# Performance work log

Measured on AMD Instinct MI355X. Metric: run time of the kernel, lower is better.

Reference implementation:

```python
import jax, jax.numpy as jnp
import numpy as np

B, T, D = 64, 1024, 512          # batch, tokens, embedding_dim
K = 2048                         # num_embeddings (codebook size)
COMMITMENT_COST = 0.25


def setup_inputs() -> dict:
    key = jax.random.key(0)
    k_in, k_w = jax.random.split(key)
    inputs = jax.random.normal(k_in, (B, T, D), dtype=jnp.float32)
    w = jax.random.normal(k_w, (K, D), dtype=jnp.float32)  # codebook buffer _w
    return {"inputs": inputs, "w": w}


def reference(inputs, w):
    input_shape = inputs.shape
    flat = inputs.reshape(-1, w.shape[1])                     # [N, D]
    distances = (jnp.sum(flat * flat, axis=1, keepdims=True)
                 + jnp.sum(w * w, axis=1)
                 - 2.0 * flat @ w.T)
    encoding_indices = jnp.argmin(distances, axis=1)          # [N]
    quantized = jnp.take(w, encoding_indices, axis=0).reshape(input_shape)

    # perplexity from hard assignment histogram (equiv. to mean of one-hot encodings)
    n = flat.shape[0]
    counts = jnp.zeros((w.shape[0],), dtype=jnp.float32).at[encoding_indices].add(1.0)
    avg_probs = counts / n
    perplexity = jnp.exp(-jnp.sum(avg_probs * jnp.log(avg_probs + 1e-10)))

    # commitment loss: mse(stop_grad(quantized), inputs) * cost
    q_sg = jax.lax.stop_gradient(quantized)
    loss = jnp.mean((q_sg - inputs) ** 2) * COMMITMENT_COST

    # straight-through estimator
    quantized_st = inputs + jax.lax.stop_gradient(quantized - inputs)
    return loss, quantized_st, perplexity, encoding_indices[:, None]
```

## Files before the change

### kernel.cpp

```cpp
#include <hip/hip_runtime.h>
#include <hip/hip_fp16.h>
#include <cmath>

#define NROWS  65536
#define DIM    512
#define KCODES 2048
#define NDTOT  33554432LL
#define MARGIN_P 0.0635f

typedef __attribute__((ext_vector_type(8))) _Float16 f16x8;
typedef __attribute__((ext_vector_type(4))) float f32x4;

#define KINS3(K1,K2,K3,V) do {                       \
    unsigned int _v = (V);                           \
    unsigned int _h1 = max((K1), _v); (K1) = min((K1), _v); \
    unsigned int _h2 = max((K2), _h1); (K2) = min((K2), _h1); \
    (K3) = min((K3), _h2);                           \
} while (0)

#define MRG3(A1,A2,A3,B1,B2,B3) do {                               \
    unsigned int _x1 = min((A1),(B1)), _y1 = max((A1),(B1));       \
    unsigned int _x2 = min((A2),(B2)), _y2 = max((A2),(B2));       \
    unsigned int _x3 = min((A3),(B3));                             \
    (A1) = _x1; (A2) = min(_y1,_x2);                               \
    (A3) = min(max(_y1,_x2), min(_x3,_y2));                        \
} while (0)

#define FDEC(K) (__uint_as_float(0x44800000u | ((((K) >> 11) & 0x1FFFFFu) << 2)) - 1024.f)

__global__ __launch_bounds__(256) void k_prepw(const float* __restrict__ src,
                                               char* __restrict__ dst,
                                               float* __restrict__ norms) {
    long gid = (long)blockIdx.x * 256 + threadIdx.x;
    int c  = (int)(gid >> 6);
    int k8 = (int)(gid & 63);
    const float4* s = (const float4*)(src + (size_t)c * DIM + k8 * 8);
    float4 v0 = s[0], v1 = s[1];
    float vv[8] = {v0.x, v0.y, v0.z, v0.w, v1.x, v1.y, v1.z, v1.w};
    unsigned int hw[4];
    float nrm = 0.f;
    #pragma unroll
    for (int j = 0; j < 4; ++j) {
        unsigned int h0 = __half_as_ushort(__float2half_rn(vv[2*j]));
        unsigned int h1 = __half_as_ushort(__float2half_rn(vv[2*j+1]));
        hw[j] = h0 | (h1 << 16);
        nrm = fmaf(vv[2*j], vv[2*j], nrm);
        nrm = fmaf(vv[2*j+1], vv[2*j+1], nrm);
    }
    int cb = c >> 8, fcol = (c >> 4) & 15;
    int ks32 = k8 >> 2, sub = k8 & 3;
    int l = sub * 16 + (c & 15);
    size_t off = (size_t)((cb * 16 + ks32) * 16 + fcol) * 1024 + (size_t)l * 16;
    *(uint4*)(dst + off) = make_uint4(hw[0], hw[1], hw[2], hw[3]);
    #pragma unroll
    for (int o = 32; o; o >>= 1) nrm += __shfl_xor(nrm, o, 64);
    if ((threadIdx.x & 63) == 0) norms[c] = nrm;
}

#define EPI(CB) do {                                                         \
    _Pragma("unroll") for (int fc = 0; fc < 4; ++fc) {                       \
        unsigned int col = (unsigned)((CB) * 256 + wc * 64 + fc * 16 + (lane & 15)); \
        float wnb = wnorm[col] + 1024.f;                                     \
        _Pragma("unroll") for (int fr = 0; fr < 4; ++fr) {                   \
            _Pragma("unroll") for (int reg = 0; reg < 4; ++reg) {            \
                float kd = fmaf(-2.f, acc[fr][fc][reg], wnb);                \
                unsigned int key = ((__float_as_uint(kd) << 9) & 0xFFFFF800u) | col; \
                int s = fr * 4 + reg;                                        \
                KINS3(k1[s], k2[s], k3[s], key);                             \
            }                                                                \
            acc[fr][fc] = (f32x4){0.f, 0.f, 0.f, 0.f};                       \
        }                                                                    \
    }                                                                        \
} while (0)

#define GSTEP(T, CUR0, CUR1, CUR2, CUR3, NXT0, NXT1, NXT2, NXT3) do {        \
    {                                                                        \
        const char* _n = wp + ((size_t)((T) + 1) << 14) + (size_t)(wc * 4) * 1024 + (size_t)lane * 16; \
        NXT0 = *(const f16x8*)(_n);                                          \
        NXT1 = *(const f16x8*)(_n + 1024);                                   \
        NXT2 = *(const f16x8*)(_n + 2048);                                   \
        NXT3 = *(const f16x8*)(_n + 3072);                                   \
    }                                                                        \
    {                                                                        \
        int _ks = (T) & 15;                                                  \
        unsigned _ab = (unsigned)((wr * 64 + (lane & 15)) * 1024 + _ks * 64  \
                                  + ((lane >> 4) << 4));                     \
        _ab ^= (unsigned)((lane & 7) << 4);                                  \
        const char* _a = smem + _ab;                                         \
        f16x8 _a0 = *(const f16x8*)(_a);                                     \
        f16x8 _a1 = *(const f16x8*)(_a + 16384);                             \
        f16x8 _a2 = *(const f16x8*)(_a + 32768);                             \
        f16x8 _a3 = *(const f16x8*)(_a + 49152);                             \
        acc[0][0] = __builtin_amdgcn_mfma_f32_16x16x32_f16(_a0, CUR0, acc[0][0], 0, 0, 0); \
        acc[1][0] = __builtin_amdgcn_mfma_f32_16x16x32_f16(_a1, CUR0, acc[1][0], 0, 0, 0); \
        acc[2][0] = __builtin_amdgcn_mfma_f32_16x16x32_f16(_a2, CUR0, acc[2][0], 0, 0, 0); \
        acc[3][0] = __builtin_amdgcn_mfma_f32_16x16x32_f16(_a3, CUR0, acc[3][0], 0, 0, 0); \
        acc[0][1] = __builtin_amdgcn_mfma_f32_16x16x32_f16(_a0, CUR1, acc[0][1], 0, 0, 0); \
        acc[1][1] = __builtin_amdgcn_mfma_f32_16x16x32_f16(_a1, CUR1, acc[1][1], 0, 0, 0); \
        acc[2][1] = __builtin_amdgcn_mfma_f32_16x16x32_f16(_a2, CUR1, acc[2][1], 0, 0, 0); \
        acc[3][1] = __builtin_amdgcn_mfma_f32_16x16x32_f16(_a3, CUR1, acc[3][1], 0, 0, 0); \
        acc[0][2] = __builtin_amdgcn_mfma_f32_16x16x32_f16(_a0, CUR2, acc[0][2], 0, 0, 0); \
        acc[1][2] = __builtin_amdgcn_mfma_f32_16x16x32_f16(_a1, CUR2, acc[1][2], 0, 0, 0); \
        acc[2][2] = __builtin_amdgcn_mfma_f32_16x16x32_f16(_a2, CUR2, acc[2][2], 0, 0, 0); \
        acc[3][2] = __builtin_amdgcn_mfma_f32_16x16x32_f16(_a3, CUR2, acc[3][2], 0, 0, 0); \
        acc[0][3] = __builtin_amdgcn_mfma_f32_16x16x32_f16(_a0, CUR3, acc[0][3], 0, 0, 0); \
        acc[1][3] = __builtin_amdgcn_mfma_f32_16x16x32_f16(_a1, CUR3, acc[1][3], 0, 0, 0); \
        acc[2][3] = __builtin_amdgcn_mfma_f32_16x16x32_f16(_a2, CUR3, acc[2][3], 0, 0, 0); \
        acc[3][3] = __builtin_amdgcn_mfma_f32_16x16x32_f16(_a3, CUR3, acc[3][3], 0, 0, 0); \
    }                                                                        \
    if (((T) & 15) == 15) EPI((T) >> 4);                                     \
} while (0)

__global__ __launch_bounds__(512, 1) void k_gemm(const float* __restrict__ x,
                                                 const char* __restrict__ wp,
                                                 const float* __restrict__ wnorm,
                                                 float* __restrict__ xnorm,
                                                 int* __restrict__ idxo,
                                                 int* __restrict__ cand2o,
                                                 int* __restrict__ cand3o,
                                                 float* __restrict__ bestd) {
    __shared__ char smem[131072];
    const int tid = threadIdx.x;
    const int lane = tid & 63;
    const int wid = tid >> 6;
    const int wr = wid >> 2, wc = wid & 3;
    const int rb = blockIdx.x;

    f32x4 acc[4][4];
    #pragma unroll
    for (int i = 0; i < 4; ++i)
        #pragma unroll
        for (int j = 0; j < 4; ++j) acc[i][j] = (f32x4){0.f, 0.f, 0.f, 0.f};

    unsigned int k1[16], k2[16], k3[16];
    #pragma unroll
    for (int s = 0; s < 16; ++s) { k1[s] = k2[s] = k3[s] = 0xFFFFFFFFu; }

    const float* xs = x + (size_t)rb * 128 * DIM;
    #pragma unroll
    for (int pass = 0; pass < 16; ++pass) {
        int row = pass * 8 + wid;
        const float4* src = (const float4*)(xs + (size_t)row * DIM) + lane * 2;
        float4 u0 = src[0], u1 = src[1];
        unsigned int p0 = (unsigned int)__half_as_ushort(__float2half_rn(u0.x))
                        | ((unsigned int)__half_as_ushort(__float2half_rn(u0.y)) << 16);
        unsigned int p1 = (unsigned int)__half_as_ushort(__float2half_rn(u0.z))
                        | ((unsigned int)__half_as_ushort(__float2half_rn(u0.w)) << 16);
        unsigned int p2 = (unsigned int)__half_as_ushort(__float2half_rn(u1.x))
                        | ((unsigned int)__half_as_ushort(__float2half_rn(u1.y)) << 16);
        unsigned int p3 = (unsigned int)__half_as_ushort(__float2half_rn(u1.z))
                        | ((unsigned int)__half_as_ushort(__float2half_rn(u1.w)) << 16);
        unsigned int addr = (unsigned int)(row * 1024 + lane * 16);
        addr ^= (unsigned int)((row & 7) << 4);
        *(uint4*)(smem + addr) = make_uint4(p0, p1, p2, p3);
        float nr = u0.x * u0.x;
        nr = fmaf(u0.y, u0.y, nr); nr = fmaf(u0.z, u0.z, nr); nr = fmaf(u0.w, u0.w, nr);
        nr = fmaf(u1.x, u1.x, nr); nr = fmaf(u1.y, u1.y, nr);
        nr = fmaf(u1.z, u1.z, nr); nr = fmaf(u1.w, u1.w, nr);
        #pragma unroll
        for (int o = 32; o; o >>= 1) nr += __shfl_xor(nr, o, 64);
        if (lane == 0) xnorm[rb * 128 + row] = nr;
    }
    f16x8 b0_0, b0_1, b0_2, b0_3, b1_0, b1_1, b1_2, b1_3;
    {
        const char* n0 = wp + (size_t)(wc * 4) * 1024 + (size_t)lane * 16;
        b0_0 = *(const f16x8*)(n0);
        b0_1 = *(const f16x8*)(n0 + 1024);
        b0_2 = *(const f16x8*)(n0 + 2048);
        b0_3 = *(const f16x8*)(n0 + 3072);
    }
    __syncthreads();

    for (int t = 0; t < 128; t += 2) {
        GSTEP(t,     b0_0, b0_1, b0_2, b0_3, b1_0, b1_1, b1_2, b1_3);
        GSTEP(t + 1, b1_0, b1_1, b1_2, b1_3, b0_0, b0_1, b0_2, b0_3);
    }

    #pragma unroll
    for (int s = 0; s < 16; ++s) {
        #pragma unroll
        for (int off = 1; off < 16; off <<= 1) {
            unsigned int b1 = (unsigned)__shfl_xor((int)k1[s], off, 16);
            unsigned int b2 = (unsigned)__shfl_xor((int)k2[s], off, 16);
            unsigned int b3 = (unsigned)__shfl_xor((int)k3[s], off, 16);
            MRG3(k1[s], k2[s], k3[s], b1, b2, b3);
        }
    }
    unsigned int m1 = 0, m2 = 0, m3 = 0;
    #pragma unroll
    for (int s = 0; s < 16; ++s) {
        bool mine = (lane & 15) == s;
        m1 = mine ? k1[s] : m1;
        m2 = mine ? k2[s] : m2;
        m3 = mine ? k3[s] : m3;
    }
    int sl = lane & 15;
    int rowl = wr * 64 + (sl >> 2) * 16 + (lane >> 4) * 4 + (sl & 3);
    __syncthreads();
    ((uint4*)smem)[rowl * 4 + wc] = make_uint4(m1, m2, m3, 0u);
    __syncthreads();
    if (tid < 128) {
        uint4 a = ((const uint4*)smem)[tid * 4 + 0];
        uint4 b = ((const uint4*)smem)[tid * 4 + 1];
        uint4 c = ((const uint4*)smem)[tid * 4 + 2];
        uint4 d = ((const uint4*)smem)[tid * 4 + 3];
        unsigned int K1 = a.x, K2 = a.y, K3 = a.z;
        MRG3(K1, K2, K3, b.x, b.y, b.z);
        MRG3(K1, K2, K3, c.x, c.y, c.z);
        MRG3(K1, K2, K3, d.x, d.y, d.z);
        float f1 = FDEC(K1);
        float f2 = FDEC(K2);
        float f3 = FDEC(K3);
        int row = rb * 128 + tid;
        idxo[row]   = (int)(K1 & 0x7FFu);
        bestd[row]  = f1;
        cand2o[row] = (f2 - f1 < MARGIN_P) ? (int)(K2 & 0x7FFu) : -1;
        cand3o[row] = (f3 - f1 < MARGIN_P) ? (int)(K3 & 0x7FFu) : -1;
    }
}

__global__ __launch_bounds__(256) void k_gather2(const float* __restrict__ x,
                                                 const float* __restrict__ w,
                                                 const int* __restrict__ idxo,
                                                 const int* __restrict__ cand2o,
                                                 const int* __restrict__ cand3o,
                                                 const float* __restrict__ bestd,
                                                 const float* __restrict__ xnorm,
                                                 float* __restrict__ out,
                                                 int* __restrict__ hist,
                                                 double* __restrict__ part) {
    __shared__ double red[4];
    int wid = threadIdx.x >> 6, lane = threadIdx.x & 63;
    int n = blockIdx.x * 4 + wid;
    int c1 = idxo[n];
    int c2 = cand2o[n];
    int cfin = c1;
    double dist = (double)bestd[n];
    if (c2 >= 0) {
        int c3 = cand3o[n];
        int c3e = (c3 < 0) ? c1 : c3;
        const float* xr = x + (size_t)n * DIM;
        const float* w1 = w + (size_t)c1 * DIM;
        const float* w2 = w + (size_t)c2 * DIM;
        const float* w3 = w + (size_t)c3e * DIM;
        double s1 = 0.0, s2 = 0.0, s3 = 0.0;
        #pragma unroll
        for (int j = 0; j < DIM / 64; ++j) {
            int d = lane + 64 * j;
            double xv = (double)xr[d];
            double a = (double)w1[d], b = (double)w2[d], c = (double)w3[d];
            s1 += a * a - 2.0 * xv * a;
            s2 += b * b - 2.0 * xv * b;
            s3 += c * c - 2.0 * xv * c;
        }
        #pragma unroll
        for (int off = 32; off; off >>= 1) {
            s1 += __shfl_xor(s1, off, 64);
            s2 += __shfl_xor(s2, off, 64);
            s3 += __shfl_xor(s3, off, 64);
        }
        double bs = s1; int bi = c1;
        if (s2 < bs || (s2 == bs && c2 < bi)) { bs = s2; bi = c2; }
        if (c3 >= 0 && (s3 < bs || (s3 == bs && c3 < bi))) { bs = s3; bi = c3; }
        cfin = bi;
        dist = bs;
    }
    const float* wq = w + (size_t)cfin * DIM;
    float* oq = out + 1 + (size_t)n * DIM;
    #pragma unroll
    for (int j = 0; j < DIM / 64; ++j) {
        int d = j * 64 + lane;
        oq[d] = wq[d];
    }
    if (lane == 0) {
        red[wid] = dist + (double)xnorm[n];
        atomicAdd(&hist[cfin], 1);
        out[2 + NDTOT + n] = (float)cfin;
    }
    __syncthreads();
    if (threadIdx.x == 0)
        part[blockIdx.x] = red[0] + red[1] + red[2] + red[3];
}

__global__ __launch_bounds__(256) void k_final2(const double* __restrict__ part,
                                                const int* __restrict__ hist,
                                                float* __restrict__ out) {
    __shared__ double sm[256];
    int t = threadIdx.x;
    double s = 0.0;
    for (int i = t; i < NROWS / 4; i += 256) s += part[i];
    sm[t] = s; __syncthreads();
    for (int off = 128; off; off >>= 1) { if (t < off) sm[t] += sm[t + off]; __syncthreads(); }
    if (t == 0) out[0] = (float)(sm[0] * 0.25 / (double)NDTOT);
    __syncthreads();
    double e = 0.0;
    for (int k = t; k < KCODES; k += 256) {
        double p = (double)hist[k] / (double)NROWS;
        e -= p * log(p + 1e-10);
    }
    sm[t] = e; __syncthreads();
    for (int off = 128; off; off >>= 1) { if (t < off) sm[t] += sm[t + off]; __syncthreads(); }
    if (t == 0) out[1 + NDTOT] = (float)exp(sm[0]);
}

extern "C" void kernel_launch(void* const* d_in, const int* in_sizes, int n_in,
                              void* d_out, int out_size, void* d_ws, size_t ws_size,
                              hipStream_t stream) {
    const float* x = (const float*)d_in[0];
    const float* w = (const float*)d_in[1];
    float* out = (float*)d_out;
    char* ws = (char*)d_ws;

    char*   wp    = ws;
    float*  wnorm = (float*)(ws + 2113536);
    int*    idxo  = (int*)(ws + 2121728);
    int*    cand2 = (int*)(ws + 2383872);
    int*    cand3 = (int*)(ws + 2646016);
    int*    hist  = (int*)(ws + 2908160);
    float*  xnorm = (float*)(ws + 2916352);
    float*  bestd = (float*)(ws + 3178496);
    double* part  = (double*)(ws + 3440640);

    hipMemsetAsync(hist, 0, KCODES * sizeof(int), stream);
    k_prepw  <<<(KCODES * 64) / 256, 256, 0, stream>>>(w, wp, wnorm);
    k_gemm   <<<NROWS / 128, 512, 0, stream>>>(x, wp, wnorm, xnorm, idxo, cand2, cand3, bestd);
    k_gather2<<<NROWS / 4, 256, 0, stream>>>(x, w, idxo, cand2, cand3, bestd, xnorm, out, hist, part);
    k_final2 <<<1, 256, 0, stream>>>(part, hist, out);
}
```

Baseline: 236.8 us.

## Use 16 waves per GEMM block with fragment-ordered LDS layout for inputs

The distance GEMM block grows from 8 to 16 waves (2x8 grid), and each wave now computes a 64x32 tile instead of 64x64, which halves its accumulator registers. Input rows are staged to LDS in an MFMA-fragment-ready layout, so the XOR swizzle is no longer needed. Row norms are reduced through a padded LDS scratch area. The explicit double-buffered prefetch of codebook fragments is dropped in favour of plain loads with unroll 4, and the final top-3 merge now combines 8 column-wave partials. The aim is more waves for latency hiding, at the cost of more LDS traffic per MFMA, a larger LDS footprint and reliance on the compiler to schedule the global loads.

```diff
diff --git a/kernel.cpp b/kernel.cpp
--- a/kernel.cpp
+++ b/kernel.cpp
@@ -57,91 +57,40 @@
     if ((threadIdx.x & 63) == 0) norms[c] = nrm;
 }
 
-#define EPI(CB) do {                                                         \
-    _Pragma("unroll") for (int fc = 0; fc < 4; ++fc) {                       \
-        unsigned int col = (unsigned)((CB) * 256 + wc * 64 + fc * 16 + (lane & 15)); \
-        float wnb = wnorm[col] + 1024.f;                                     \
-        _Pragma("unroll") for (int fr = 0; fr < 4; ++fr) {                   \
-            _Pragma("unroll") for (int reg = 0; reg < 4; ++reg) {            \
-                float kd = fmaf(-2.f, acc[fr][fc][reg], wnb);                \
-                unsigned int key = ((__float_as_uint(kd) << 9) & 0xFFFFF800u) | col; \
-                int s = fr * 4 + reg;                                        \
-                KINS3(k1[s], k2[s], k3[s], key);                             \
-            }                                                                \
-            acc[fr][fc] = (f32x4){0.f, 0.f, 0.f, 0.f};                       \
-        }                                                                    \
-    }                                                                        \
-} while (0)
-
-#define GSTEP(T, CUR0, CUR1, CUR2, CUR3, NXT0, NXT1, NXT2, NXT3) do {        \
-    {                                                                        \
-        const char* _n = wp + ((size_t)((T) + 1) << 14) + (size_t)(wc * 4) * 1024 + (size_t)lane * 16; \
-        NXT0 = *(const f16x8*)(_n);                                          \
-        NXT1 = *(const f16x8*)(_n + 1024);                                   \
-        NXT2 = *(const f16x8*)(_n + 2048);                                   \
-        NXT3 = *(const f16x8*)(_n + 3072);                                   \
-    }                                                                        \
-    {                                                                        \
-        int _ks = (T) & 15;                                                  \
-        unsigned _ab = (unsigned)((wr * 64 + (lane & 15)) * 1024 + _ks * 64  \
-                                  + ((lane >> 4) << 4));                     \
-        _ab ^= (unsigned)((lane & 7) << 4);                                  \
-        const char* _a = smem + _ab;                                         \
-        f16x8 _a0 = *(const f16x8*)(_a);                                     \
-        f16x8 _a1 = *(const f16x8*)(_a + 16384);                             \
-        f16x8 _a2 = *(const f16x8*)(_a + 32768);                             \
-        f16x8 _a3 = *(const f16x8*)(_a + 49152);                             \
-        acc[0][0] = __builtin_amdgcn_mfma_f32_16x16x32_f16(_a0, CUR0, acc[0][0], 0, 0, 0); \
-        acc[1][0] = __builtin_amdgcn_mfma_f32_16x16x32_f16(_a1, CUR0, acc[1][0], 0, 0, 0); \
-        acc[2][0] = __builtin_amdgcn_mfma_f32_16x16x32_f16(_a2, CUR0, acc[2][0], 0, 0, 0); \
-        acc[3][0] = __builtin_amdgcn_mfma_f32_16x16x32_f16(_a3, CUR0, acc[3][0], 0, 0, 0); \
-        acc[0][1] = __builtin_amdgcn_mfma_f32_16x16x32_f16(_a0, CUR1, acc[0][1], 0, 0, 0); \
-        acc[1][1] = __builtin_amdgcn_mfma_f32_16x16x32_f16(_a1, CUR1, acc[1][1], 0, 0, 0); \
-        acc[2][1] = __builtin_amdgcn_mfma_f32_16x16x32_f16(_a2, CUR1, acc[2][1], 0, 0, 0); \
-        acc[3][1] = __builtin_amdgcn_mfma_f32_16x16x32_f16(_a3, CUR1, acc[3][1], 0, 0, 0); \
-        acc[0][2] = __builtin_amdgcn_mfma_f32_16x16x32_f16(_a0, CUR2, acc[0][2], 0, 0, 0); \
-        acc[1][2] = __builtin_amdgcn_mfma_f32_16x16x32_f16(_a1, CUR2, acc[1][2], 0, 0, 0); \
-        acc[2][2] = __builtin_amdgcn_mfma_f32_16x16x32_f16(_a2, CUR2, acc[2][2], 0, 0, 0); \
-        acc[3][2] = __builtin_amdgcn_mfma_f32_16x16x32_f16(_a3, CUR2, acc[3][2], 0, 0, 0); \
-        acc[0][3] = __builtin_amdgcn_mfma_f32_16x16x32_f16(_a0, CUR3, acc[0][3], 0, 0, 0); \
-        acc[1][3] = __builtin_amdgcn_mfma_f32_16x16x32_f16(_a1, CUR3, acc[1][3], 0, 0, 0); \
-        acc[2][3] = __builtin_amdgcn_mfma_f32_16x16x32_f16(_a2, CUR3, acc[2][3], 0, 0, 0); \
-        acc[3][3] = __builtin_amdgcn_mfma_f32_16x16x32_f16(_a3, CUR3, acc[3][3], 0, 0, 0); \
-    }                                                                        \
-    if (((T) & 15) == 15) EPI((T) >> 4);                                     \
-} while (0)
-
-__global__ __launch_bounds__(512, 1) void k_gemm(const float* __restrict__ x,
-                                                 const char* __restrict__ wp,
-                                                 const float* __restrict__ wnorm,
-                                                 float* __restrict__ xnorm,
-                                                 int* __restrict__ idxo,
-                                                 int* __restrict__ cand2o,
-                                                 int* __restrict__ cand3o,
-                                                 float* __restrict__ bestd) {
-    __shared__ char smem[131072];
+__global__ __launch_bounds__(1024, 1) void k_gemm(const float* __restrict__ x,
+                                                  const char* __restrict__ wp,
+                                                  const float* __restrict__ wnorm,
+                                                  float* __restrict__ xnorm,
+                                                  int* __restrict__ idxo,
+                                                  int* __restrict__ cand2o,
+                                                  int* __restrict__ cand3o,
+                                                  float* __restrict__ bestd) {
+    __shared__ char smem[139776];
     const int tid = threadIdx.x;
     const int lane = tid & 63;
     const int wid = tid >> 6;
-    const int wr = wid >> 2, wc = wid & 3;
+    const int wr = wid >> 3, wc = wid & 7;
     const int rb = blockIdx.x;
-
-    f32x4 acc[4][4];
+    float* pn = (float*)(smem + 131072);
+
+    f32x4 acc[4][2];
     #pragma unroll
     for (int i = 0; i < 4; ++i)
         #pragma unroll
-        for (int j = 0; j < 4; ++j) acc[i][j] = (f32x4){0.f, 0.f, 0.f, 0.f};
+        for (int j = 0; j < 2; ++j) acc[i][j] = (f32x4){0.f, 0.f, 0.f, 0.f};
 
     unsigned int k1[16], k2[16], k3[16];
     #pragma unroll
     for (int s = 0; s < 16; ++s) { k1[s] = k2[s] = k3[s] = 0xFFFFFFFFu; }
 
     const float* xs = x + (size_t)rb * 128 * DIM;
-    #pragma unroll
-    for (int pass = 0; pass < 16; ++pass) {
-        int row = pass * 8 + wid;
-        const float4* src = (const float4*)(xs + (size_t)row * DIM) + lane * 2;
-        float4 u0 = src[0], u1 = src[1];
+    const unsigned chunkbase = (unsigned)((wid >> 1) * 16384 + (wid & 1) * 8192);
+    #pragma unroll
+    for (int frow = 0; frow < 8; ++frow) {
+        int row = frow * 16 + (lane & 15);
+        const float* src = xs + (size_t)row * DIM + wid * 32 + (lane >> 4) * 8;
+        float4 u0 = *(const float4*)(src);
+        float4 u1 = *(const float4*)(src + 4);
         unsigned int p0 = (unsigned int)__half_as_ushort(__float2half_rn(u0.x))
                         | ((unsigned int)__half_as_ushort(__float2half_rn(u0.y)) << 16);
         unsigned int p1 = (unsigned int)__half_as_ushort(__float2half_rn(u0.z))
@@ -150,30 +99,62 @@
                         | ((unsigned int)__half_as_ushort(__float2half_rn(u1.y)) << 16);
         unsigned int p3 = (unsigned int)__half_as_ushort(__float2half_rn(u1.z))
                         | ((unsigned int)__half_as_ushort(__float2half_rn(u1.w)) << 16);
-        unsigned int addr = (unsigned int)(row * 1024 + lane * 16);
-        addr ^= (unsigned int)((row & 7) << 4);
-        *(uint4*)(smem + addr) = make_uint4(p0, p1, p2, p3);
+        *(uint4*)(smem + chunkbase + frow * 1024 + lane * 16) = make_uint4(p0, p1, p2, p3);
         float nr = u0.x * u0.x;
         nr = fmaf(u0.y, u0.y, nr); nr = fmaf(u0.z, u0.z, nr); nr = fmaf(u0.w, u0.w, nr);
         nr = fmaf(u1.x, u1.x, nr); nr = fmaf(u1.y, u1.y, nr);
         nr = fmaf(u1.z, u1.z, nr); nr = fmaf(u1.w, u1.w, nr);
-        #pragma unroll
-        for (int o = 32; o; o >>= 1) nr += __shfl_xor(nr, o, 64);
-        if (lane == 0) xnorm[rb * 128 + row] = nr;
-    }
-    f16x8 b0_0, b0_1, b0_2, b0_3, b1_0, b1_1, b1_2, b1_3;
-    {
-        const char* n0 = wp + (size_t)(wc * 4) * 1024 + (size_t)lane * 16;
-        b0_0 = *(const f16x8*)(n0);
-        b0_1 = *(const f16x8*)(n0 + 1024);
-        b0_2 = *(const f16x8*)(n0 + 2048);
-        b0_3 = *(const f16x8*)(n0 + 3072);
-    }
-    __syncthreads();
-
-    for (int t = 0; t < 128; t += 2) {
-        GSTEP(t,     b0_0, b0_1, b0_2, b0_3, b1_0, b1_1, b1_2, b1_3);
-        GSTEP(t + 1, b1_0, b1_1, b1_2, b1_3, b0_0, b0_1, b0_2, b0_3);
+        nr += __shfl_xor(nr, 16, 64);
+        nr += __shfl_xor(nr, 32, 64);
+        if (lane < 16) pn[row * 17 + wid] = nr;
+    }
+    __syncthreads();
+    if (tid < 128) {
+        float s = 0.f;
+        #pragma unroll
+        for (int j = 0; j < 16; ++j) s += pn[tid * 17 + j];
+        xnorm[rb * 128 + tid] = s;
+    }
+
+    for (int cb = 0; cb < 8; ++cb) {
+        #pragma unroll 4
+        for (int ks = 0; ks < 16; ++ks) {
+            int t = cb * 16 + ks;
+            const char* bp = wp + ((size_t)t << 14) + (size_t)(wc * 2) * 1024
+                           + (size_t)lane * 16;
+            f16x8 b0 = *(const f16x8*)(bp);
+            f16x8 b1 = *(const f16x8*)(bp + 1024);
+            const char* a = smem + (ks >> 1) * 16384 + (ks & 1) * 8192
+                          + (wr * 4) * 1024 + lane * 16;
+            f16x8 a0 = *(const f16x8*)(a);
+            f16x8 a1 = *(const f16x8*)(a + 1024);
+            f16x8 a2 = *(const f16x8*)(a + 2048);
+            f16x8 a3 = *(const f16x8*)(a + 3072);
+            acc[0][0] = __builtin_amdgcn_mfma_f32_16x16x32_f16(a0, b0, acc[0][0], 0, 0, 0);
+            acc[1][0] = __builtin_amdgcn_mfma_f32_16x16x32_f16(a1, b0, acc[1][0], 0, 0, 0);
+            acc[2][0] = __builtin_amdgcn_mfma_f32_16x16x32_f16(a2, b0, acc[2][0], 0, 0, 0);
+            acc[3][0] = __builtin_amdgcn_mfma_f32_16x16x32_f16(a3, b0, acc[3][0], 0, 0, 0);
+            acc[0][1] = __builtin_amdgcn_mfma_f32_16x16x32_f16(a0, b1, acc[0][1], 0, 0, 0);
+            acc[1][1] = __builtin_amdgcn_mfma_f32_16x16x32_f16(a1, b1, acc[1][1], 0, 0, 0);
+            acc[2][1] = __builtin_amdgcn_mfma_f32_16x16x32_f16(a2, b1, acc[2][1], 0, 0, 0);
+            acc[3][1] = __builtin_amdgcn_mfma_f32_16x16x32_f16(a3, b1, acc[3][1], 0, 0, 0);
+        }
+        #pragma unroll
+        for (int fc = 0; fc < 2; ++fc) {
+            unsigned int col = (unsigned)(cb * 256 + wc * 32 + fc * 16 + (lane & 15));
+            float wnb = wnorm[col] + 1024.f;
+            #pragma unroll
+            for (int fr = 0; fr < 4; ++fr) {
+                #pragma unroll
+                for (int reg = 0; reg < 4; ++reg) {
+                    float kd = fmaf(-2.f, acc[fr][fc][reg], wnb);
+                    unsigned int key = ((__float_as_uint(kd) << 9) & 0xFFFFF800u) | col;
+                    int s = fr * 4 + reg;
+                    KINS3(k1[s], k2[s], k3[s], key);
+                }
+                acc[fr][fc] = (f32x4){0.f, 0.f, 0.f, 0.f};
+            }
+        }
     }
 
     #pragma unroll
@@ -197,17 +178,17 @@
     int sl = lane & 15;
     int rowl = wr * 64 + (sl >> 2) * 16 + (lane >> 4) * 4 + (sl & 3);
     __syncthreads();
-    ((uint4*)smem)[rowl * 4 + wc] = make_uint4(m1, m2, m3, 0u);
+    ((uint4*)smem)[rowl * 8 + wc] = make_uint4(m1, m2, m3, 0u);
     __syncthreads();
     if (tid < 128) {
-        uint4 a = ((const uint4*)smem)[tid * 4 + 0];
-        uint4 b = ((const uint4*)smem)[tid * 4 + 1];
-        uint4 c = ((const uint4*)smem)[tid * 4 + 2];
-        uint4 d = ((const uint4*)smem)[tid * 4 + 3];
-        unsigned int K1 = a.x, K2 = a.y, K3 = a.z;
-        MRG3(K1, K2, K3, b.x, b.y, b.z);
-        MRG3(K1, K2, K3, c.x, c.y, c.z);
-        MRG3(K1, K2, K3, d.x, d.y, d.z);
+        const uint4* e = (const uint4*)smem + tid * 8;
+        uint4 e0 = e[0];
+        unsigned int K1 = e0.x, K2 = e0.y, K3 = e0.z;
+        #pragma unroll
+        for (int j = 1; j < 8; ++j) {
+            uint4 ej = e[j];
+            MRG3(K1, K2, K3, ej.x, ej.y, ej.z);
+        }
         float f1 = FDEC(K1);
         float f2 = FDEC(K2);
         float f3 = FDEC(K3);
@@ -323,7 +304,7 @@
 
     hipMemsetAsync(hist, 0, KCODES * sizeof(int), stream);
     k_prepw  <<<(KCODES * 64) / 256, 256, 0, stream>>>(w, wp, wnorm);
-    k_gemm   <<<NROWS / 128, 512, 0, stream>>>(x, wp, wnorm, xnorm, idxo, cand2, cand3, bestd);
+    k_gemm   <<<NROWS / 128, 1024, 0, stream>>>(x, wp, wnorm, xnorm, idxo, cand2, cand3, bestd);
     k_gather2<<<NROWS / 4, 256, 0, stream>>>(x, w, idxo, cand2, cand3, bestd, xnorm, out, hist, part);
     k_final2 <<<1, 256, 0, stream>>>(part, hist, out);
 }
```

New measurement: 223.4 us (median of 3 runs). -5.7%, faster.

## Store x tile in MFMA-fragment-major LDS layout for contiguous A loads

Applied to the files above, without the earlier changes.

The fp16 input tile in shared memory moves from a row-major swizzled layout to one ordered by MFMA fragment, so each wave reads its A operands as contiguous 16-byte-per-lane chunks without XOR address arithmetic. The staging loop now has each wave own a K slice across all rows, and row norms become per-wave partial sums written to a padded shared array, then reduced by 128 threads after the barrier. The B pointer base is hoisted out of the step macro. The cost is extra shared memory for the partial norms, one more reduction step after the barrier, and a less coalesced global read pattern for x.

```diff
diff --git a/kernel.cpp b/kernel.cpp
--- a/kernel.cpp
+++ b/kernel.cpp
@@ -75,7 +75,7 @@
 
 #define GSTEP(T, CUR0, CUR1, CUR2, CUR3, NXT0, NXT1, NXT2, NXT3) do {        \
     {                                                                        \
-        const char* _n = wp + ((size_t)((T) + 1) << 14) + (size_t)(wc * 4) * 1024 + (size_t)lane * 16; \
+        const char* _n = bbase + ((size_t)((T) + 1) << 14);                  \
         NXT0 = *(const f16x8*)(_n);                                          \
         NXT1 = *(const f16x8*)(_n + 1024);                                   \
         NXT2 = *(const f16x8*)(_n + 2048);                                   \
@@ -83,14 +83,12 @@
     }                                                                        \
     {                                                                        \
         int _ks = (T) & 15;                                                  \
-        unsigned _ab = (unsigned)((wr * 64 + (lane & 15)) * 1024 + _ks * 64  \
-                                  + ((lane >> 4) << 4));                     \
-        _ab ^= (unsigned)((lane & 7) << 4);                                  \
-        const char* _a = smem + _ab;                                         \
+        const char* _a = smem + (_ks >> 1) * 16384 + (_ks & 1) * 8192        \
+                       + (wr * 4) * 1024 + lane * 16;                        \
         f16x8 _a0 = *(const f16x8*)(_a);                                     \
-        f16x8 _a1 = *(const f16x8*)(_a + 16384);                             \
-        f16x8 _a2 = *(const f16x8*)(_a + 32768);                             \
-        f16x8 _a3 = *(const f16x8*)(_a + 49152);                             \
+        f16x8 _a1 = *(const f16x8*)(_a + 1024);                              \
+        f16x8 _a2 = *(const f16x8*)(_a + 2048);                              \
+        f16x8 _a3 = *(const f16x8*)(_a + 3072);                              \
         acc[0][0] = __builtin_amdgcn_mfma_f32_16x16x32_f16(_a0, CUR0, acc[0][0], 0, 0, 0); \
         acc[1][0] = __builtin_amdgcn_mfma_f32_16x16x32_f16(_a1, CUR0, acc[1][0], 0, 0, 0); \
         acc[2][0] = __builtin_amdgcn_mfma_f32_16x16x32_f16(_a2, CUR0, acc[2][0], 0, 0, 0); \
@@ -119,12 +117,13 @@
                                                  int* __restrict__ cand2o,
                                                  int* __restrict__ cand3o,
                                                  float* __restrict__ bestd) {
-    __shared__ char smem[131072];
+    __shared__ char smem[135680];
     const int tid = threadIdx.x;
     const int lane = tid & 63;
     const int wid = tid >> 6;
     const int wr = wid >> 2, wc = wid & 3;
     const int rb = blockIdx.x;
+    float* pn = (float*)(smem + 131072);
 
     f32x4 acc[4][4];
     #pragma unroll
@@ -138,42 +137,50 @@
 
     const float* xs = x + (size_t)rb * 128 * DIM;
     #pragma unroll
-    for (int pass = 0; pass < 16; ++pass) {
-        int row = pass * 8 + wid;
-        const float4* src = (const float4*)(xs + (size_t)row * DIM) + lane * 2;
-        float4 u0 = src[0], u1 = src[1];
-        unsigned int p0 = (unsigned int)__half_as_ushort(__float2half_rn(u0.x))
-                        | ((unsigned int)__half_as_ushort(__float2half_rn(u0.y)) << 16);
-        unsigned int p1 = (unsigned int)__half_as_ushort(__float2half_rn(u0.z))
-                        | ((unsigned int)__half_as_ushort(__float2half_rn(u0.w)) << 16);
-        unsigned int p2 = (unsigned int)__half_as_ushort(__float2half_rn(u1.x))
-                        | ((unsigned int)__half_as_ushort(__float2half_rn(u1.y)) << 16);
-        unsigned int p3 = (unsigned int)__half_as_ushort(__float2half_rn(u1.z))
-                        | ((unsigned int)__half_as_ushort(__float2half_rn(u1.w)) << 16);
-        unsigned int addr = (unsigned int)(row * 1024 + lane * 16);
-        addr ^= (unsigned int)((row & 7) << 4);
-        *(uint4*)(smem + addr) = make_uint4(p0, p1, p2, p3);
-        float nr = u0.x * u0.x;
-        nr = fmaf(u0.y, u0.y, nr); nr = fmaf(u0.z, u0.z, nr); nr = fmaf(u0.w, u0.w, nr);
-        nr = fmaf(u1.x, u1.x, nr); nr = fmaf(u1.y, u1.y, nr);
-        nr = fmaf(u1.z, u1.z, nr); nr = fmaf(u1.w, u1.w, nr);
-        #pragma unroll
-        for (int o = 32; o; o >>= 1) nr += __shfl_xor(nr, o, 64);
-        if (lane == 0) xnorm[rb * 128 + row] = nr;
-    }
-    f16x8 b0_0, b0_1, b0_2, b0_3, b1_0, b1_1, b1_2, b1_3;
-    {
-        const char* n0 = wp + (size_t)(wc * 4) * 1024 + (size_t)lane * 16;
-        b0_0 = *(const f16x8*)(n0);
-        b0_1 = *(const f16x8*)(n0 + 1024);
-        b0_2 = *(const f16x8*)(n0 + 2048);
-        b0_3 = *(const f16x8*)(n0 + 3072);
-    }
-    __syncthreads();
+    for (int frow = 0; frow < 8; ++frow) {
+        int row = frow * 16 + (lane & 15);
+        float nr = 0.f;
+        #pragma unroll
+        for (int ksub = 0; ksub < 2; ++ksub) {
+            const float* src = xs + (size_t)row * DIM + wid * 64 + ksub * 32 + (lane >> 4) * 8;
+            float4 u0 = *(const float4*)(src);
+            float4 u1 = *(const float4*)(src + 4);
+            unsigned int p0 = (unsigned int)__half_as_ushort(__float2half_rn(u0.x))
+                            | ((unsigned int)__half_as_ushort(__float2half_rn(u0.y)) << 16);
+            unsigned int p1 = (unsigned int)__half_as_ushort(__float2half_rn(u0.z))
+                            | ((unsigned int)__half_as_ushort(__float2half_rn(u0.w)) << 16);
+            unsigned int p2 = (unsigned int)__half_as_ushort(__float2half_rn(u1.x))
+                            | ((unsigned int)__half_as_ushort(__float2half_rn(u1.y)) << 16);
+            unsigned int p3 = (unsigned int)__half_as_ushort(__float2half_rn(u1.z))
+                            | ((unsigned int)__half_as_ushort(__float2half_rn(u1.w)) << 16);
+            *(uint4*)(smem + wid * 16384 + ksub * 8192 + frow * 1024 + lane * 16)
+                = make_uint4(p0, p1, p2, p3);
+            nr = fmaf(u0.x, u0.x, nr); nr = fmaf(u0.y, u0.y, nr);
+            nr = fmaf(u0.z, u0.z, nr); nr = fmaf(u0.w, u0.w, nr);
+            nr = fmaf(u1.x, u1.x, nr); nr = fmaf(u1.y, u1.y, nr);
+            nr = fmaf(u1.z, u1.z, nr); nr = fmaf(u1.w, u1.w, nr);
+        }
+        nr += __shfl_xor(nr, 16, 64);
+        nr += __shfl_xor(nr, 32, 64);
+        if (lane < 16) pn[row * 9 + wid] = nr;
+    }
+    const char* bbase = wp + (size_t)(wc * 4) * 1024 + (size_t)lane * 16;
+    f16x8 bc0, bc1, bc2, bc3, bn0, bn1, bn2, bn3;
+    bc0 = *(const f16x8*)(bbase);
+    bc1 = *(const f16x8*)(bbase + 1024);
+    bc2 = *(const f16x8*)(bbase + 2048);
+    bc3 = *(const f16x8*)(bbase + 3072);
+    __syncthreads();
+    if (tid < 128) {
+        float s = 0.f;
+        #pragma unroll
+        for (int j = 0; j < 8; ++j) s += pn[tid * 9 + j];
+        xnorm[rb * 128 + tid] = s;
+    }
 
     for (int t = 0; t < 128; t += 2) {
-        GSTEP(t,     b0_0, b0_1, b0_2, b0_3, b1_0, b1_1, b1_2, b1_3);
-        GSTEP(t + 1, b1_0, b1_1, b1_2, b1_3, b0_0, b0_1, b0_2, b0_3);
+        GSTEP(t,     bc0, bc1, bc2, bc3, bn0, bn1, bn2, bn3);
+        GSTEP(t + 1, bn0, bn1, bn2, bn3, bc0, bc1, bc2, bc3);
     }
 
     #pragma unroll
```

Measured after the change: 236.0 us. No clear change (-0.3%).
